# Optimization experiments

Hardware: AMD Instinct MI355X
Metric: run time of the kernel (lower is better)

The kernel has to match this reference:

```python
import jax, jax.numpy as jnp
import numpy as np

EMBED_DIM = 1024
NUM_HEADS = 16
HEAD_DIM = EMBED_DIM // NUM_HEADS
WINDOW_SIZE = 256
BATCH = 2
SEQ = 2048


def setup_inputs() -> dict:
    key = jax.random.key(0)
    ks = jax.random.split(key, 5)
    s = 1.0 / np.sqrt(EMBED_DIM)
    return {
        "x": jax.random.normal(ks[0], (BATCH, SEQ, EMBED_DIM), dtype=jnp.float32),
        "Wq": jax.random.normal(ks[1], (EMBED_DIM, EMBED_DIM), dtype=jnp.float32) * s,
        "Wk": jax.random.normal(ks[2], (EMBED_DIM, EMBED_DIM), dtype=jnp.float32) * s,
        "Wv": jax.random.normal(ks[3], (EMBED_DIM, EMBED_DIM), dtype=jnp.float32) * s,
        "Wo": jax.random.normal(ks[4], (EMBED_DIM, EMBED_DIM), dtype=jnp.float32) * s,
    }


def _split_heads(t):
    # [B, S, E] -> [B, H, S, D]
    b, s, _ = t.shape
    return t.reshape(b, s, NUM_HEADS, HEAD_DIM).transpose(0, 2, 1, 3)


def reference(x, Wq, Wk, Wv, Wo):
    b, s, _ = x.shape
    # nn.Linear(bias=False): y = x @ W.T
    q = _split_heads(x @ Wq.T)
    k = _split_heads(x @ Wk.T)
    v = _split_heads(x @ Wv.T)
    scores = jnp.einsum("bhqd,bhkd->bhqk", q, k) / np.sqrt(HEAD_DIM).astype(np.float32)
    i = jnp.arange(s)[:, None]
    j = jnp.arange(s)[None, :]
    # causal sliding window: attend to j in [i - window_size + 1, i]
    allowed = (j <= i) & (j >= i - WINDOW_SIZE + 1)
    scores = jnp.where(allowed[None, None], scores, -jnp.inf)
    probs = jax.nn.softmax(scores, axis=-1)
    ctx = jnp.einsum("bhqk,bhkd->bhqd", probs, v)  # [B,H,S,D]
    ctx = ctx.transpose(0, 2, 1, 3).reshape(b, s, EMBED_DIM)
    return ctx @ Wo.T
```

## Files before the change

kernel.cpp:

```cpp
#include <hip/hip_runtime.h>
#include <hip/hip_bf16.h>
#include <stdint.h>

#define EDIM 1024
#define NH 16
#define HD 64
#define WIN 256
#define BB 2
#define SS 2048
#define MR (BB*SS)
#define NQKV 3072

typedef __attribute__((ext_vector_type(8))) short short8;
typedef __attribute__((ext_vector_type(4))) short short4v;
typedef __attribute__((ext_vector_type(4))) float f32x4;

__device__ __forceinline__ unsigned short f2bf(float f) {
  union { float f; uint32_t u; } c; c.f = f;
  uint32_t r = (c.u + 0x7FFFu + ((c.u >> 16) & 1u)) >> 16;
  return (unsigned short)r;
}

__global__ __launch_bounds__(256) void cvt_all(const float* __restrict__ x,
                                               const float* __restrict__ Wq,
                                               const float* __restrict__ Wk,
                                               const float* __restrict__ Wv,
                                               const float* __restrict__ Wo,
                                               unsigned short* __restrict__ dst) {
  const int i = blockIdx.x * 256 + threadIdx.x;
  const float* s; int off;
  if (i < 524288) { s = x; off = i; }
  else {
    const int j = i - 524288, wsel = j >> 17;
    off = j & 131071;
    s = wsel == 0 ? Wq : wsel == 1 ? Wk : wsel == 2 ? Wv : Wo;
  }
  const float4* s4 = (const float4*)s;
  float4 a = s4[2*off], b = s4[2*off+1];
  short8 o;
  o[0]=(short)f2bf(a.x); o[1]=(short)f2bf(a.y); o[2]=(short)f2bf(a.z); o[3]=(short)f2bf(a.w);
  o[4]=(short)f2bf(b.x); o[5]=(short)f2bf(b.y); o[6]=(short)f2bf(b.z); o[7]=(short)f2bf(b.w);
  ((short8*)dst)[i] = o;
}

template<typename OutT, int BM, int BN>
__global__ __launch_bounds__(256) void gemm_bt(const unsigned short* __restrict__ A,
                                               const unsigned short* __restrict__ Bw,
                                               OutT* __restrict__ C,
                                               int M, int N, int K, int nbx) {
  constexpr int MI = BM / 32;
  constexpr int NI = BN / 32;
  constexpr int LA = BM / 32;
  constexpr int LB = BN / 32;
  __shared__ unsigned short As[BM * 64];
  __shared__ unsigned short Bs[BN * 64];
  const int t = threadIdx.x, lane = t & 63;
  const int w = t >> 6, wr = w >> 1, wc = w & 1;
  const int nwg = gridDim.x, bid = blockIdx.x;
  const int wg = (bid & 7) * (nwg >> 3) + (bid >> 3);
  const int m0 = (wg / nbx) * BM, n0 = (wg % nbx) * BN;
  f32x4 acc[MI][NI] = {};
  for (int kt = 0; kt < K; kt += 64) {
    __syncthreads();
#pragma unroll
    for (int r = 0; r < LA; ++r) {
      const int row = r*32 + (t >> 3);
      const int colb = (((t & 7) ^ (row & 7)) << 4);
      const int o = r*4096 + t*16;
      __builtin_amdgcn_global_load_lds(
        (const __attribute__((address_space(1))) char*)(A + (size_t)(m0 + row) * K + kt + (colb >> 1)),
        (__attribute__((address_space(3))) char*)((char*)As + o), 16, 0, 0);
    }
#pragma unroll
    for (int r = 0; r < LB; ++r) {
      const int row = r*32 + (t >> 3);
      const int colb = (((t & 7) ^ (row & 7)) << 4);
      const int o = r*4096 + t*16;
      __builtin_amdgcn_global_load_lds(
        (const __attribute__((address_space(1))) char*)(Bw + (size_t)(n0 + row) * K + kt + (colb >> 1)),
        (__attribute__((address_space(3))) char*)((char*)Bs + o), 16, 0, 0);
    }
    __syncthreads();
#pragma unroll
    for (int c = 0; c < 2; ++c) {
      const int k0 = c*32 + ((lane >> 4) << 3);
      short8 af[MI], bfr[NI];
#pragma unroll
      for (int mi = 0; mi < MI; ++mi) {
        const int row = wr*(BM/2) + mi*16 + (lane & 15);
        const int off = ((row << 7) + (k0 << 1)) ^ ((row & 7) << 4);
        af[mi] = *(const short8*)((const char*)As + off);
      }
#pragma unroll
      for (int ni = 0; ni < NI; ++ni) {
        const int row = wc*(BN/2) + ni*16 + (lane & 15);
        const int off = ((row << 7) + (k0 << 1)) ^ ((row & 7) << 4);
        bfr[ni] = *(const short8*)((const char*)Bs + off);
      }
#pragma unroll
      for (int mi = 0; mi < MI; ++mi)
#pragma unroll
        for (int ni = 0; ni < NI; ++ni)
          acc[mi][ni] = __builtin_amdgcn_mfma_f32_16x16x32_bf16(af[mi], bfr[ni], acc[mi][ni], 0, 0, 0);
    }
  }
#pragma unroll
  for (int mi = 0; mi < MI; ++mi) {
    const int rb = m0 + wr*(BM/2) + mi*16 + ((lane >> 4) << 2);
#pragma unroll
    for (int ni = 0; ni < NI; ++ni) {
      const int col = n0 + wc*(BN/2) + ni*16 + (lane & 15);
#pragma unroll
      for (int reg = 0; reg < 4; ++reg) {
        const float v = acc[mi][ni][reg];
        const size_t idx = (size_t)(rb + reg) * N + col;
        if constexpr (sizeof(OutT) == 2) ((unsigned short*)C)[idx] = f2bf(v);
        else ((float*)C)[idx] = v;
      }
    }
  }
}

__global__ __launch_bounds__(256) void attn_kernel(const unsigned short* __restrict__ qkv,
                                                   unsigned short* __restrict__ ctx) {
  __shared__ __align__(16) unsigned short Ks[64*64];
  __shared__ __align__(16) unsigned short VTs[64*64];
  __shared__ __align__(16) unsigned short Ps[4][16*64];
  const int t = threadIdx.x, lane = t & 63, w = t >> 6;
  const int bid = blockIdx.x;
  const int swz = (bid & 7) * 128 + (bid >> 3);
  const int qt = swz & 31, bh = swz >> 5;
  const int b = bh >> 4, h = bh & 15;
  const int q0 = qt << 6;
  const int qw0 = q0 + (w << 4);
  const unsigned short* qb = qkv + (size_t)b * SS * NQKV + h * HD;
  const unsigned short* kb = qb + EDIM;
  const unsigned short* vb = qb + 2*EDIM;
  short8 aq[2];
  {
    const size_t roff = (size_t)(qw0 + (lane & 15)) * NQKV + ((lane >> 4) << 3);
    aq[0] = *(const short8*)(qb + roff);
    aq[1] = *(const short8*)(qb + roff + 32);
  }
  const unsigned vt0 = (unsigned)(uintptr_t)(__attribute__((address_space(3))) char*)((char*)VTs);
  const unsigned trbase = vt0 + ((lane & 15) << 3) + ((lane >> 4) << 7);
  f32x4 oacc[4] = {};
  float mrun[4], lrun[4];
#pragma unroll
  for (int r = 0; r < 4; ++r) { mrun[r] = -1e30f; lrun[r] = 0.f; }
  const int t_lo = qt >= 4 ? qt - 4 : 0;
  for (int kt = t_lo; kt <= qt; ++kt) {
    const int kv0 = kt << 6;
    __syncthreads();
#pragma unroll
    for (int r = 0; r < 2; ++r) {
      const int o = r*4096 + t*16;
      const int key = o >> 7;
      const int colb = (o & 127) ^ ((key & 7) << 4);
      __builtin_amdgcn_global_load_lds(
        (const __attribute__((address_space(1))) char*)(kb + (size_t)(kv0 + key) * NQKV + (colb >> 1)),
        (__attribute__((address_space(3))) char*)((char*)Ks + o), 16, 0, 0);
    }
#pragma unroll
    for (int i = 0; i < 2; ++i) {
      const int p8 = (w << 6) + lane + (i << 8);
      const int band = p8 >> 7, rr = p8 & 127, ordv = rr >> 3, q8 = rr & 7;
      const int k = ((ordv & 7) << 3) + ((ordv >> 3) << 2) + (q8 >> 1);
      const int d = (band << 4) + ((q8 & 1) << 3);
      __builtin_amdgcn_global_load_lds(
        (const __attribute__((address_space(1))) char*)(vb + (size_t)(kv0 + k) * NQKV + d),
        (__attribute__((address_space(3))) char*)((char*)VTs + p8*16), 16, 0, 0);
    }
    __syncthreads();
    f32x4 sc[4] = {};
    __builtin_amdgcn_s_setprio(1);
#pragma unroll
    for (int kf = 0; kf < 4; ++kf) {
#pragma unroll
      for (int c = 0; c < 2; ++c) {
        const int krow = (kf << 4) + (lane & 15);
        const int k0 = (c << 5) + ((lane >> 4) << 3);
        const int off = ((krow << 7) + (k0 << 1)) ^ ((krow & 7) << 4);
        short8 bk = *(const short8*)((const char*)Ks + off);
        sc[kf] = __builtin_amdgcn_mfma_f32_16x16x32_bf16(aq[c], bk, sc[kf], 0, 0, 0);
      }
    }
    __builtin_amdgcn_s_setprio(0);
#pragma unroll
    for (int reg = 0; reg < 4; ++reg) {
      const int qg = qw0 + ((lane >> 4) << 2) + reg;
      float sv[4];
#pragma unroll
      for (int kf = 0; kf < 4; ++kf) {
        const int kg = kv0 + (kf << 4) + (lane & 15);
        const bool ok = (kg <= qg) && (kg + WIN > qg);
        sv[kf] = ok ? sc[kf][reg] * 0.125f : -1e30f;
      }
      float pm = fmaxf(fmaxf(sv[0], sv[1]), fmaxf(sv[2], sv[3]));
      pm = fmaxf(pm, __shfl_xor(pm, 1));
      pm = fmaxf(pm, __shfl_xor(pm, 2));
      pm = fmaxf(pm, __shfl_xor(pm, 4));
      pm = fmaxf(pm, __shfl_xor(pm, 8));
      const float mn = fmaxf(mrun[reg], pm);
      const float corr = __expf(mrun[reg] - mn);
      mrun[reg] = mn;
      float rs = 0.f;
      const int qrow = ((lane >> 4) << 2) + reg;
#pragma unroll
      for (int kf = 0; kf < 4; ++kf) {
        const float p = __expf(sv[kf] - mn);
        rs += p;
        const int key = (kf << 4) + (lane & 15);
        const int off = ((qrow << 7) + (key << 1)) ^ ((qrow & 7) << 4);
        *(unsigned short*)((char*)&Ps[w][0] + off) = f2bf(p);
      }
      rs += __shfl_xor(rs, 1);
      rs += __shfl_xor(rs, 2);
      rs += __shfl_xor(rs, 4);
      rs += __shfl_xor(rs, 8);
      lrun[reg] = lrun[reg] * corr + rs;
#pragma unroll
      for (int nf = 0; nf < 4; ++nf) oacc[nf][reg] *= corr;
    }
#pragma unroll
    for (int c2 = 0; c2 < 2; ++c2) {
      const int prow = lane & 15;
      const int k0 = (c2 << 5) + ((lane >> 4) << 3);
      const int offp = ((prow << 7) + (k0 << 1)) ^ ((prow & 7) << 4);
      short8 pa = *(const short8*)((const char*)&Ps[w][0] + offp);
      short4v lo[4], hi[4];
#pragma unroll
      for (int nf = 0; nf < 4; ++nf) {
        const unsigned a1 = trbase + (nf << 11) + (c2 << 9);
        asm volatile("ds_read_b64_tr_b16 %0, %1" : "=&v"(lo[nf]) : "v"(a1));
        asm volatile("ds_read_b64_tr_b16 %0, %1 offset:1024" : "=&v"(hi[nf]) : "v"(a1));
      }
      asm volatile("s_waitcnt lgkmcnt(0)" ::: "memory");
      __builtin_amdgcn_sched_barrier(0);
      __builtin_amdgcn_s_setprio(1);
#pragma unroll
      for (int nf = 0; nf < 4; ++nf) {
        short8 bv = __builtin_shufflevector(lo[nf], hi[nf], 0, 1, 2, 3, 4, 5, 6, 7);
        oacc[nf] = __builtin_amdgcn_mfma_f32_16x16x32_bf16(pa, bv, oacc[nf], 0, 0, 0);
      }
      __builtin_amdgcn_s_setprio(0);
    }
  }
  unsigned short* cb = ctx + (size_t)b * SS * EDIM + h * HD;
#pragma unroll
  for (int nf = 0; nf < 4; ++nf)
#pragma unroll
    for (int reg = 0; reg < 4; ++reg) {
      const int qg = qw0 + ((lane >> 4) << 2) + reg;
      const int d = (nf << 4) + (lane & 15);
      cb[(size_t)qg * EDIM + d] = f2bf(oacc[nf][reg] / lrun[reg]);
    }
}

extern "C" void kernel_launch(void* const* d_in, const int* in_sizes, int n_in,
                              void* d_out, int out_size, void* d_ws, size_t ws_size,
                              hipStream_t stream) {
  const float* x  = (const float*)d_in[0];
  const float* Wq = (const float*)d_in[1];
  const float* Wk = (const float*)d_in[2];
  const float* Wv = (const float*)d_in[3];
  const float* Wo = (const float*)d_in[4];
  float* out = (float*)d_out;
  char* ws = (char*)d_ws;
  unsigned short* xb   = (unsigned short*)(ws);
  unsigned short* ctxb = (unsigned short*)(ws);
  unsigned short* wqkv = (unsigned short*)(ws + (size_t)(8u << 20));
  unsigned short* wob  = (unsigned short*)(ws + (size_t)(14u << 20));
  unsigned short* qkv  = (unsigned short*)(ws + (size_t)(16u << 20));

  cvt_all<<<dim3(4096), dim3(256), 0, stream>>>(x, Wq, Wk, Wv, Wo, xb);

  gemm_bt<unsigned short, 128, 128><<<dim3(768), dim3(256), 0, stream>>>(
      xb, wqkv, qkv, MR, NQKV, EDIM, NQKV/128);

  attn_kernel<<<dim3(1024), dim3(256), 0, stream>>>(qkv, ctxb);

  gemm_bt<float, 128, 64><<<dim3(512), dim3(256), 0, stream>>>(
      ctxb, wob, out, MR, EDIM, EDIM, EDIM/64);
}
```

Measured before the change: 161.4 us.

## Replace GEMM with triple-buffered LDS ring pipeline using direct global-to-LDS loads

Rewrites both projection GEMMs to use a three-slot LDS ring with a K-step of 32. Tiles are prefetched two iterations ahead via global_load_lds, and the code waits with explicit vmcnt/lgkmcnt counts and a single s_barrier per step instead of two __syncthreads. This is meant to overlap global memory latency with MFMA work. The swizzle changes to suit 64-byte rows. The trade is more LDS per block, which may lower occupancy, plus dependence on hand-written waitcnt values and wraparound prefetches that issue redundant loads in the last two iterations.

```diff
diff --git a/kernel.cpp b/kernel.cpp
--- a/kernel.cpp
+++ b/kernel.cpp
@@ -1,6 +1,7 @@
 #include <hip/hip_runtime.h>
 #include <hip/hip_bf16.h>
 #include <stdint.h>
+
 
 #define EDIM 1024
 #define NH 16
@@ -19,6 +20,13 @@
   union { float f; uint32_t u; } c; c.f = f;
   uint32_t r = (c.u + 0x7FFFu + ((c.u >> 16) & 1u)) >> 16;
   return (unsigned short)r;
+}
+
+template<int N> __device__ __forceinline__ void wait_vm_lgkm0() {
+  if constexpr (N == 3) asm volatile("s_waitcnt vmcnt(3) lgkmcnt(0)" ::: "memory");
+  else if constexpr (N == 4) asm volatile("s_waitcnt vmcnt(4) lgkmcnt(0)" ::: "memory");
+  else if constexpr (N == 6) asm volatile("s_waitcnt vmcnt(6) lgkmcnt(0)" ::: "memory");
+  else asm volatile("s_waitcnt vmcnt(0) lgkmcnt(0)" ::: "memory");
 }
 
 __global__ __launch_bounds__(256) void cvt_all(const float* __restrict__ x,
@@ -43,73 +51,90 @@
   ((short8*)dst)[i] = o;
 }
 
-template<typename OutT, int BM, int BN>
-__global__ __launch_bounds__(256) void gemm_bt(const unsigned short* __restrict__ A,
-                                               const unsigned short* __restrict__ Bw,
-                                               OutT* __restrict__ C,
-                                               int M, int N, int K, int nbx) {
-  constexpr int MI = BM / 32;
-  constexpr int NI = BN / 32;
-  constexpr int LA = BM / 32;
-  constexpr int LB = BN / 32;
-  __shared__ unsigned short As[BM * 64];
-  __shared__ unsigned short Bs[BN * 64];
+template<typename OutT, int BM, int BN, int WM, int WN>
+__global__ __launch_bounds__(WM*WN*64) void gemm_ring(const unsigned short* __restrict__ A,
+                                                      const unsigned short* __restrict__ Bw,
+                                                      OutT* __restrict__ C,
+                                                      int M, int N, int K, int nbx) {
+  constexpr int NT = WM * WN * 64;
+  constexpr int MI = BM / (WM * 16);
+  constexpr int NI = BN / (WN * 16);
+  constexpr int LA = (BM * 4) / NT;
+  constexpr int LB = (BN * 4) / NT;
+  constexpr int LT = LA + LB;
+  constexpr int TPB = (BM + BN) * 64;
+  __shared__ __align__(16) char smem[3 * TPB];
   const int t = threadIdx.x, lane = t & 63;
-  const int w = t >> 6, wr = w >> 1, wc = w & 1;
+  const int w = t >> 6, wr = w & (WM - 1), wc = w / WM;
   const int nwg = gridDim.x, bid = blockIdx.x;
   const int wg = (bid & 7) * (nwg >> 3) + (bid >> 3);
   const int m0 = (wg / nbx) * BM, n0 = (wg % nbx) * BN;
+  const int KT = K >> 5;
+
+  auto stage = [&](char* dA, char* dB, int kt) {
+#pragma unroll
+    for (int r = 0; r < LA; ++r) {
+      const int chunk = r * NT + t;
+      const int row = chunk >> 2, c = chunk & 3;
+      const int sc = c ^ ((row >> 1) & 3);
+      __builtin_amdgcn_global_load_lds(
+        (const __attribute__((address_space(1))) char*)(A + (size_t)(m0 + row) * K + kt + sc * 8),
+        (__attribute__((address_space(3))) char*)(dA + chunk * 16), 16, 0, 0);
+    }
+#pragma unroll
+    for (int r = 0; r < LB; ++r) {
+      const int chunk = r * NT + t;
+      const int row = chunk >> 2, c = chunk & 3;
+      const int sc = c ^ ((row >> 1) & 3);
+      __builtin_amdgcn_global_load_lds(
+        (const __attribute__((address_space(1))) char*)(Bw + (size_t)(n0 + row) * K + kt + sc * 8),
+        (__attribute__((address_space(3))) char*)(dB + chunk * 16), 16, 0, 0);
+    }
+  };
+
   f32x4 acc[MI][NI] = {};
-  for (int kt = 0; kt < K; kt += 64) {
-    __syncthreads();
-#pragma unroll
-    for (int r = 0; r < LA; ++r) {
-      const int row = r*32 + (t >> 3);
-      const int colb = (((t & 7) ^ (row & 7)) << 4);
-      const int o = r*4096 + t*16;
-      __builtin_amdgcn_global_load_lds(
-        (const __attribute__((address_space(1))) char*)(A + (size_t)(m0 + row) * K + kt + (colb >> 1)),
-        (__attribute__((address_space(3))) char*)((char*)As + o), 16, 0, 0);
-    }
-#pragma unroll
-    for (int r = 0; r < LB; ++r) {
-      const int row = r*32 + (t >> 3);
-      const int colb = (((t & 7) ^ (row & 7)) << 4);
-      const int o = r*4096 + t*16;
-      __builtin_amdgcn_global_load_lds(
-        (const __attribute__((address_space(1))) char*)(Bw + (size_t)(n0 + row) * K + kt + (colb >> 1)),
-        (__attribute__((address_space(3))) char*)((char*)Bs + o), 16, 0, 0);
-    }
-    __syncthreads();
-#pragma unroll
-    for (int c = 0; c < 2; ++c) {
-      const int k0 = c*32 + ((lane >> 4) << 3);
-      short8 af[MI], bfr[NI];
-#pragma unroll
-      for (int mi = 0; mi < MI; ++mi) {
-        const int row = wr*(BM/2) + mi*16 + (lane & 15);
-        const int off = ((row << 7) + (k0 << 1)) ^ ((row & 7) << 4);
-        af[mi] = *(const short8*)((const char*)As + off);
-      }
-#pragma unroll
-      for (int ni = 0; ni < NI; ++ni) {
-        const int row = wc*(BN/2) + ni*16 + (lane & 15);
-        const int off = ((row << 7) + (k0 << 1)) ^ ((row & 7) << 4);
-        bfr[ni] = *(const short8*)((const char*)Bs + off);
-      }
-#pragma unroll
-      for (int mi = 0; mi < MI; ++mi)
-#pragma unroll
-        for (int ni = 0; ni < NI; ++ni)
-          acc[mi][ni] = __builtin_amdgcn_mfma_f32_16x16x32_bf16(af[mi], bfr[ni], acc[mi][ni], 0, 0, 0);
-    }
+  stage(smem, smem + BM * 64, 0);
+  stage(smem + TPB, smem + TPB + BM * 64, 32);
+  wait_vm_lgkm0<LT>();
+  __builtin_amdgcn_s_barrier();
+  __builtin_amdgcn_sched_barrier(0);
+
+  int cur = 0;
+  for (int tt = 0; tt < KT; ++tt) {
+    int sb = cur + 2; if (sb >= 3) sb -= 3;
+    int nt2 = tt + 2; if (nt2 >= KT) nt2 -= KT;
+    char* dA = smem + sb * TPB;
+    stage(dA, dA + BM * 64, nt2 << 5);
+    const char* rA = smem + cur * TPB;
+    const char* rB = rA + BM * 64;
+    short8 af[MI], bfr[NI];
+    const int chq = (lane >> 4);
+#pragma unroll
+    for (int mi = 0; mi < MI; ++mi) {
+      const int row = wr * (BM / WM) + mi * 16 + (lane & 15);
+      af[mi] = *(const short8*)(rA + row * 64 + ((chq ^ ((row >> 1) & 3)) << 4));
+    }
+#pragma unroll
+    for (int ni = 0; ni < NI; ++ni) {
+      const int row = wc * (BN / WN) + ni * 16 + (lane & 15);
+      bfr[ni] = *(const short8*)(rB + row * 64 + ((chq ^ ((row >> 1) & 3)) << 4));
+    }
+#pragma unroll
+    for (int mi = 0; mi < MI; ++mi)
+#pragma unroll
+      for (int ni = 0; ni < NI; ++ni)
+        acc[mi][ni] = __builtin_amdgcn_mfma_f32_16x16x32_bf16(af[mi], bfr[ni], acc[mi][ni], 0, 0, 0);
+    wait_vm_lgkm0<LT>();
+    __builtin_amdgcn_s_barrier();
+    __builtin_amdgcn_sched_barrier(0);
+    cur = cur + 1 == 3 ? 0 : cur + 1;
   }
 #pragma unroll
   for (int mi = 0; mi < MI; ++mi) {
-    const int rb = m0 + wr*(BM/2) + mi*16 + ((lane >> 4) << 2);
+    const int rb = m0 + wr * (BM / WM) + mi * 16 + ((lane >> 4) << 2);
 #pragma unroll
     for (int ni = 0; ni < NI; ++ni) {
-      const int col = n0 + wc*(BN/2) + ni*16 + (lane & 15);
+      const int col = n0 + wc * (BN / WN) + ni * 16 + (lane & 15);
 #pragma unroll
       for (int reg = 0; reg < 4; ++reg) {
         const float v = acc[mi][ni][reg];
@@ -275,11 +300,11 @@
 
   cvt_all<<<dim3(4096), dim3(256), 0, stream>>>(x, Wq, Wk, Wv, Wo, xb);
 
-  gemm_bt<unsigned short, 128, 128><<<dim3(768), dim3(256), 0, stream>>>(
+  gemm_ring<unsigned short, 128, 128, 2, 2><<<dim3(768), dim3(256), 0, stream>>>(
       xb, wqkv, qkv, MR, NQKV, EDIM, NQKV/128);
 
   attn_kernel<<<dim3(1024), dim3(256), 0, stream>>>(qkv, ctxb);
 
-  gemm_bt<float, 128, 64><<<dim3(512), dim3(256), 0, stream>>>(
+  gemm_ring<float, 128, 64, 2, 2><<<dim3(512), dim3(256), 0, stream>>>(
       ctxb, wob, out, MR, EDIM, EDIM, EDIM/64);
 }
```

New measurement: 162.5 us. About the same (+0.7%).
